# Kernel tuning notes

Measured on AMD Instinct MI355X. Metric: run time of the kernel, lower is better.

Reference implementation:

```python
import jax, jax.numpy as jnp
import numpy as np

N_NODES = 100000
N_EDGES = 1600000
IN_CH = 256
OUT_CH = 128


def setup_inputs() -> dict:
    key = jax.random.key(0)
    k1, k2, k3, k4, k5, k6 = jax.random.split(key, 6)
    x = jax.random.normal(k1, (N_NODES, IN_CH), dtype=jnp.float32)
    edge_src = jax.random.randint(k2, (N_EDGES,), 0, N_NODES, dtype=jnp.int32)
    edge_dst = jax.random.randint(k3, (N_EDGES,), 0, N_NODES, dtype=jnp.int32)
    edge_weight = jax.random.uniform(k4, (N_EDGES,), dtype=jnp.float32)
    # Linear params (torch nn.Linear: y = x @ W.T + b)
    W = jax.random.normal(k5, (OUT_CH, IN_CH), dtype=jnp.float32) * (1.0 / np.sqrt(IN_CH))
    b = jax.random.normal(k6, (OUT_CH,), dtype=jnp.float32) * 0.01
    return {"x": x, "edge_src": edge_src, "edge_dst": edge_dst,
            "edge_weight": edge_weight, "W": W, "b": b}


def reference(x, edge_src, edge_dst, edge_weight, W, b):
    # Linear projection: [N, in] -> [N, out]
    h = x @ W.T + b
    # spmm sum aggregation: out[d] = sum_{e: dst(e)=d} w_e * h[src(e)]
    msgs = h[edge_src] * edge_weight[:, None]  # [E, out]
    out = jax.ops.segment_sum(msgs, edge_dst, num_segments=N_NODES)
    return out
```

## Files before the change

### kernel.cpp

```cpp
#include <hip/hip_runtime.h>
#include <hip/hip_bf16.h>

#define IN_CH 256
#define OUT_CH 128
#define BIN_SHIFT 6
#define BIN_SIZE 64
#define MAXNB2 2048
#define CHUNK3 4096
#define NBLK_MAX 512
#define K4BATCH 1536
#define K4CAP 2048

using bf16x8 = __attribute__((ext_vector_type(8))) __bf16;
using f32x16 = __attribute__((ext_vector_type(16))) float;
using f32x4  = __attribute__((ext_vector_type(4))) float;
using f32x2  = __attribute__((ext_vector_type(2))) float;

__device__ __forceinline__ unsigned int f2bf(float f) {
    union { float f; unsigned u; } v; v.f = f;
    unsigned r = v.u + 0x7fffu + ((v.u >> 16) & 1u);
    return r >> 16;
}

__global__ void __launch_bounds__(512) k1_hist(
    const float* __restrict__ W, unsigned short* __restrict__ Wfrag,
    const int* __restrict__ edge_dst, unsigned short* __restrict__ bh,
    int n_edges, int nb2) {
    const int t = threadIdx.x;
    if (blockIdx.x < 8) {
        const int flat = blockIdx.x * 512 + t;
        const int l = flat & 63;
        const int ks = (flat >> 6) & 15;
        const int c = flat >> 10;
        const int row = c * 32 + (l & 31);
        const int col0 = ks * 16 + 8 * (l >> 5);
        const float* src = W + (size_t)row * IN_CH + col0;
        uint4 o;
        o.x = f2bf(src[0]) | (f2bf(src[1]) << 16);
        o.y = f2bf(src[2]) | (f2bf(src[3]) << 16);
        o.z = f2bf(src[4]) | (f2bf(src[5]) << 16);
        o.w = f2bf(src[6]) | (f2bf(src[7]) << 16);
        *reinterpret_cast<uint4*>(Wfrag + (size_t)flat * 8) = o;
        return;
    }
    __shared__ int hist[MAXNB2];
    const int blk = blockIdx.x - 8;
    for (int i = t; i < MAXNB2; i += 512) hist[i] = 0;
    __syncthreads();
    const int base = blk * CHUNK3;
#pragma unroll
    for (int j = 0; j < CHUNK3 / 512; ++j) {
        int e = base + j * 512 + t;
        if (e < n_edges) atomicAdd(&hist[edge_dst[e] >> BIN_SHIFT], 1);
    }
    __syncthreads();
    for (int i = t; i < nb2; i += 512) bh[(size_t)i * NBLK_MAX + blk] = (unsigned short)hist[i];
}

__global__ void __launch_bounds__(512) k2a_scan_cols(
    const unsigned short* __restrict__ bh, unsigned short* __restrict__ offs,
    int* __restrict__ total, int nblk) {
    __shared__ int sd[512];
    const int t = threadIdx.x;
    const int bin = blockIdx.x;
    int val = (t < nblk) ? (int)bh[(size_t)bin * NBLK_MAX + t] : 0;
    sd[t] = val;
    __syncthreads();
    for (int s = 1; s < 512; s <<= 1) {
        int y = (t >= s) ? sd[t - s] : 0;
        __syncthreads();
        sd[t] += y;
        __syncthreads();
    }
    offs[(size_t)bin * NBLK_MAX + t] = (unsigned short)(sd[t] - val);
    if (t == 511) total[bin] = sd[511];
}

__global__ void __launch_bounds__(512) k2b_scan_base(
    const int* __restrict__ total, int* __restrict__ base, int nb2) {
    __shared__ int sd[512];
    const int t = threadIdx.x;
    int v[4];
    int loc = 0;
#pragma unroll
    for (int k = 0; k < 4; ++k) {
        int idx = t * 4 + k;
        v[k] = (idx < nb2) ? total[idx] : 0;
        loc += v[k];
    }
    sd[t] = loc;
    __syncthreads();
    for (int s = 1; s < 512; s <<= 1) {
        int y = (t >= s) ? sd[t - s] : 0;
        __syncthreads();
        sd[t] += y;
        __syncthreads();
    }
    int run = sd[t] - loc;
#pragma unroll
    for (int k = 0; k < 4; ++k) {
        int idx = t * 4 + k;
        if (idx < nb2) base[idx] = run;
        run += v[k];
    }
    if (t == 511) base[nb2] = sd[511];
}

__global__ void __launch_bounds__(512) linear_mfma(
    const float* __restrict__ x, const unsigned short* __restrict__ Wfrag,
    const float* __restrict__ b, unsigned short* __restrict__ h, int n_nodes) {
    __shared__ uint4 wlds[4096];
    const int tid = threadIdx.x;
    const int w = tid >> 6, l = tid & 63;
    const int l31 = l & 31, lh = l >> 5;
    const int node0 = blockIdx.x * 256 + w * 32;

    {
        const uint4* wfg = reinterpret_cast<const uint4*>(Wfrag);
#pragma unroll
        for (int j = 0; j < 8; ++j) wlds[j * 512 + tid] = wfg[j * 512 + tid];
    }
    __syncthreads();

    int arow = node0 + l31;
    if (arow > n_nodes - 1) arow = n_nodes - 1;
    const float* xrow = x + (size_t)arow * IN_CH + 8 * lh;

    f32x16 acc0 = {}, acc1 = {}, acc2 = {}, acc3 = {};

#pragma unroll 4
    for (int ks = 0; ks < 16; ++ks) {
        float4 a0 = *reinterpret_cast<const float4*>(xrow + ks * 16);
        float4 a1 = *reinterpret_cast<const float4*>(xrow + ks * 16 + 4);
        bf16x8 af;
        af[0] = (__bf16)a0.x; af[1] = (__bf16)a0.y;
        af[2] = (__bf16)a0.z; af[3] = (__bf16)a0.w;
        af[4] = (__bf16)a1.x; af[5] = (__bf16)a1.y;
        af[6] = (__bf16)a1.z; af[7] = (__bf16)a1.w;

        uint4 bw0 = wlds[(0 * 16 + ks) * 64 + l];
        uint4 bw1 = wlds[(1 * 16 + ks) * 64 + l];
        uint4 bw2 = wlds[(2 * 16 + ks) * 64 + l];
        uint4 bw3 = wlds[(3 * 16 + ks) * 64 + l];

        acc0 = __builtin_amdgcn_mfma_f32_32x32x16_bf16(af, __builtin_bit_cast(bf16x8, bw0), acc0, 0, 0, 0);
        acc1 = __builtin_amdgcn_mfma_f32_32x32x16_bf16(af, __builtin_bit_cast(bf16x8, bw1), acc1, 0, 0, 0);
        acc2 = __builtin_amdgcn_mfma_f32_32x32x16_bf16(af, __builtin_bit_cast(bf16x8, bw2), acc2, 0, 0, 0);
        acc3 = __builtin_amdgcn_mfma_f32_32x32x16_bf16(af, __builtin_bit_cast(bf16x8, bw3), acc3, 0, 0, 0);
    }

    const float bias0 = b[0 + l31], bias1 = b[32 + l31], bias2 = b[64 + l31], bias3 = b[96 + l31];
#pragma unroll
    for (int reg = 0; reg < 16; ++reg) {
        const int r = (reg & 3) + 8 * (reg >> 2) + 4 * lh;
        const int node = node0 + r;
        if (node < n_nodes) {
            unsigned short* hp = h + (size_t)node * OUT_CH;
            __bf16 t0 = (__bf16)(acc0[reg] + bias0);
            __bf16 t1 = (__bf16)(acc1[reg] + bias1);
            __bf16 t2 = (__bf16)(acc2[reg] + bias2);
            __bf16 t3 = (__bf16)(acc3[reg] + bias3);
            hp[0 + l31]  = __builtin_bit_cast(unsigned short, t0);
            hp[32 + l31] = __builtin_bit_cast(unsigned short, t1);
            hp[64 + l31] = __builtin_bit_cast(unsigned short, t2);
            hp[96 + l31] = __builtin_bit_cast(unsigned short, t3);
        }
    }
}

__global__ void __launch_bounds__(512) k3_bin(
    const int* __restrict__ edge_src, const int* __restrict__ edge_dst,
    const float* __restrict__ edge_weight,
    const unsigned short* __restrict__ offs, const int* __restrict__ base,
    unsigned long long* __restrict__ records, int n_edges, int nb2) {
    __shared__ unsigned long long staged[CHUNK3];
    __shared__ int hist[MAXNB2];
    __shared__ int cur[MAXNB2];
    __shared__ int gbase[MAXNB2];
    __shared__ int sd[512];

    const int t = threadIdx.x;
    const int blk = blockIdx.x;
    const int ebase = blk * CHUNK3;
    const int count = min(CHUNK3, n_edges - ebase);

    for (int i = t; i < MAXNB2; i += 512) hist[i] = 0;
    __syncthreads();
#pragma unroll
    for (int j = 0; j < CHUNK3 / 512; ++j) {
        int e = ebase + j * 512 + t;
        if (e < n_edges) atomicAdd(&hist[edge_dst[e] >> BIN_SHIFT], 1);
    }
    __syncthreads();
    int h0 = hist[4 * t], h1 = hist[4 * t + 1], h2 = hist[4 * t + 2], h3 = hist[4 * t + 3];
    int loc = h0 + h1 + h2 + h3;
    sd[t] = loc;
    __syncthreads();
    for (int s = 1; s < 512; s <<= 1) {
        int y = (t >= s) ? sd[t - s] : 0;
        __syncthreads();
        sd[t] += y;
        __syncthreads();
    }
    int excl = sd[t] - loc;
    {
        int run = excl;
        cur[4 * t] = run; run += h0;
        cur[4 * t + 1] = run; run += h1;
        cur[4 * t + 2] = run; run += h2;
        cur[4 * t + 3] = run;
    }
    {
        int run = excl;
#pragma unroll
        for (int k = 0; k < 4; ++k) {
            int bin = 4 * t + k;
            if (bin < nb2)
                gbase[bin] = base[bin] + (int)offs[(size_t)bin * NBLK_MAX + blk] - run;
            run += (k == 0 ? h0 : k == 1 ? h1 : k == 2 ? h2 : h3);
        }
    }
    __syncthreads();
#pragma unroll
    for (int j = 0; j < CHUNK3 / 512; ++j) {
        int e = ebase + j * 512 + t;
        if (e < n_edges) {
            int d = edge_dst[e];
            int bin = d >> BIN_SHIFT;
            unsigned int wbits = f2bf(edge_weight[e]);
            unsigned long long rec = ((unsigned long long)wbits << 48) |
                                     ((unsigned long long)bin << 24) |
                                     ((unsigned long long)(d & (BIN_SIZE - 1)) << 17) |
                                     (unsigned int)edge_src[e];
            int pos = atomicAdd(&cur[bin], 1);
            staged[pos] = rec;
        }
    }
    __syncthreads();
    for (int i = t; i < count; i += 512) {
        unsigned long long r = staged[i];
        int bin = (int)((r >> 24) & 4095u);
        records[gbase[bin] + i] = r;
    }
}

__global__ void __launch_bounds__(256) k4_agg(
    const unsigned short* __restrict__ h, const unsigned long long* __restrict__ records,
    const int* __restrict__ base, float* __restrict__ out, int n_nodes) {
    __shared__ unsigned long long sorted[K4CAP];
    __shared__ int hist[BIN_SIZE];
    __shared__ int cur[BIN_SIZE];
    __shared__ int pstart[BIN_SIZE];
    __shared__ int sd[BIN_SIZE];
    __shared__ int ptot;

    const int t = threadIdx.x;
    const int bin = blockIdx.x;
    const int w = t >> 6, lane = t & 63;
    const int rbeg = base[bin], rend = base[bin + 1];

    float acc[16][2];
#pragma unroll
    for (int d = 0; d < 16; ++d) { acc[d][0] = 0.f; acc[d][1] = 0.f; }

    for (int b0 = rbeg; b0 < rend; b0 += K4BATCH) {
        const int cnt = min(K4BATCH, rend - b0);
        __syncthreads();
        if (t < BIN_SIZE) hist[t] = 0;
        __syncthreads();
        for (int i = t; i < cnt; i += 256)
            atomicAdd(&hist[(unsigned)(records[b0 + i] >> 17) & 63u], 1);
        __syncthreads();
        if (t < BIN_SIZE) sd[t] = (hist[t] + 7) & ~7;
        __syncthreads();
        for (int s = 1; s < BIN_SIZE; s <<= 1) {
            int y = 0;
            if (t < BIN_SIZE && t >= s) y = sd[t - s];
            __syncthreads();
            if (t < BIN_SIZE) sd[t] += y;
            __syncthreads();
        }
        if (t < BIN_SIZE) {
            const int e = sd[t] - ((hist[t] + 7) & ~7);
            pstart[t] = e;
            cur[t] = e;
        }
        if (t == BIN_SIZE - 1) ptot = sd[BIN_SIZE - 1];
        __syncthreads();
        const int pt = ptot;
        for (int i = t; i < pt; i += 256) sorted[i] = 0ull;
        __syncthreads();
        for (int i = t; i < cnt; i += 256) {
            const unsigned long long r = records[b0 + i];
            const int dl = (int)((unsigned)(r >> 17) & 63u);
            const int pos = atomicAdd(&cur[dl], 1);
            sorted[pos] = r;
        }
        __syncthreads();
#pragma unroll
        for (int d = 0; d < 16; ++d) {
            const int dl = w * 16 + d;
            const int s0 = pstart[dl];
            const int s1 = s0 + hist[dl];
            float a0 = 0.f, a1 = 0.f;
            for (int i = s0; i < s1; i += 8) {
                unsigned int hv[8];
                float wt[8];
#pragma unroll
                for (int j = 0; j < 8; ++j) {
                    const unsigned long long rr = sorted[i + j];
                    const unsigned lo = __builtin_amdgcn_readfirstlane((unsigned)rr);
                    const unsigned hi = __builtin_amdgcn_readfirstlane((unsigned)(rr >> 32));
                    wt[j] = __builtin_bit_cast(float, hi & 0xFFFF0000u);
                    const unsigned* hp = reinterpret_cast<const unsigned*>(
                        h + (size_t)(lo & 0x1FFFFu) * OUT_CH);
                    hv[j] = hp[lane];
                }
#pragma unroll
                for (int j = 0; j < 8; ++j) {
                    a0 += wt[j] * __builtin_bit_cast(float, hv[j] << 16);
                    a1 += wt[j] * __builtin_bit_cast(float, hv[j] & 0xFFFF0000u);
                }
            }
            acc[d][0] += a0;
            acc[d][1] += a1;
        }
    }

#pragma unroll
    for (int d = 0; d < 16; ++d) {
        const int node = bin * BIN_SIZE + w * 16 + d;
        if (node < n_nodes) {
            f32x2 v = {acc[d][0], acc[d][1]};
            __builtin_nontemporal_store(
                v, reinterpret_cast<f32x2*>(out + (size_t)node * OUT_CH + 2 * lane));
        }
    }
}

extern "C" void kernel_launch(void* const* d_in, const int* in_sizes, int n_in,
                              void* d_out, int out_size, void* d_ws, size_t ws_size,
                              hipStream_t stream) {
    const float* x           = (const float*)d_in[0];
    const int*   edge_src    = (const int*)d_in[1];
    const int*   edge_dst    = (const int*)d_in[2];
    const float* edge_weight = (const float*)d_in[3];
    const float* W           = (const float*)d_in[4];
    const float* b           = (const float*)d_in[5];
    float* out = (float*)d_out;

    const int n_nodes = in_sizes[0] / IN_CH;
    const int n_edges = in_sizes[1];
    const int nb2 = (n_nodes + BIN_SIZE - 1) / BIN_SIZE;
    const int nblk = (n_edges + CHUNK3 - 1) / CHUNK3;

    unsigned long long* records = (unsigned long long*)d_ws;
    unsigned short* h     = (unsigned short*)(records + n_edges);
    unsigned short* bh    = (unsigned short*)(h + (size_t)n_nodes * OUT_CH);
    unsigned short* offs  = bh + (size_t)MAXNB2 * NBLK_MAX;
    int* total = (int*)(offs + (size_t)MAXNB2 * NBLK_MAX);
    int* base  = total + MAXNB2;
    unsigned short* Wfrag = (unsigned short*)(base + MAXNB2 + 2);

    k1_hist<<<8 + nblk, 512, 0, stream>>>(W, Wfrag, edge_dst, bh, n_edges, nb2);
    k2a_scan_cols<<<nb2, 512, 0, stream>>>(bh, offs, total, nblk);
    k2b_scan_base<<<1, 512, 0, stream>>>(total, base, nb2);
    linear_mfma<<<(n_nodes + 255) / 256, 512, 0, stream>>>(x, Wfrag, b, h, n_nodes);
    k3_bin<<<nblk, 512, 0, stream>>>(edge_src, edge_dst, edge_weight,
                                     offs, base, records, n_edges, nb2);
    k4_agg<<<nb2, 256, 0, stream>>>(h, records, base, out, n_nodes);
}
```

Before: 135.6 us.

## Merge edge binning and linear projection into one heterogeneous launch; stage records in LDS

The edge-binning kernel and the MFMA linear projection become one launch, with the block index choosing which role a block plays. Both roles share a 64KB LDS buffer. The aim is to remove a launch boundary and let the memory-bound scatter overlap with the GEMM. Separately, the aggregation kernel now copies each record batch into LDS once instead of reading it from global memory twice. The trade-off is higher LDS use per block, which could lower occupancy.

```diff
diff --git a/kernel.cpp b/kernel.cpp
--- a/kernel.cpp
+++ b/kernel.cpp
@@ -106,19 +106,97 @@
     if (t == 511) base[nb2] = sd[511];
 }
 
-__global__ void __launch_bounds__(512) linear_mfma(
+__global__ void __launch_bounds__(512) k3_linear(
+    const int* __restrict__ edge_src, const int* __restrict__ edge_dst,
+    const float* __restrict__ edge_weight,
+    const unsigned short* __restrict__ offs, const int* __restrict__ base,
+    unsigned long long* __restrict__ records, int n_edges, int nb2, int nblk,
     const float* __restrict__ x, const unsigned short* __restrict__ Wfrag,
     const float* __restrict__ b, unsigned short* __restrict__ h, int n_nodes) {
-    __shared__ uint4 wlds[4096];
-    const int tid = threadIdx.x;
-    const int w = tid >> 6, l = tid & 63;
+    __shared__ __align__(16) char smem[65536];
+    const int t = threadIdx.x;
+
+    if ((int)blockIdx.x < nblk) {
+        unsigned long long* staged = (unsigned long long*)smem;
+        int* hist  = (int*)(smem + 32768);
+        int* cur   = (int*)(smem + 40960);
+        int* gbase = (int*)(smem + 49152);
+        int* sd    = (int*)(smem + 57344);
+
+        const int blk = blockIdx.x;
+        const int ebase = blk * CHUNK3;
+        const int count = min(CHUNK3, n_edges - ebase);
+
+        for (int i = t; i < MAXNB2; i += 512) hist[i] = 0;
+        __syncthreads();
+#pragma unroll
+        for (int j = 0; j < CHUNK3 / 512; ++j) {
+            int e = ebase + j * 512 + t;
+            if (e < n_edges) atomicAdd(&hist[edge_dst[e] >> BIN_SHIFT], 1);
+        }
+        __syncthreads();
+        int h0 = hist[4 * t], h1 = hist[4 * t + 1], h2 = hist[4 * t + 2], h3 = hist[4 * t + 3];
+        int loc = h0 + h1 + h2 + h3;
+        sd[t] = loc;
+        __syncthreads();
+        for (int s = 1; s < 512; s <<= 1) {
+            int y = (t >= s) ? sd[t - s] : 0;
+            __syncthreads();
+            sd[t] += y;
+            __syncthreads();
+        }
+        int excl = sd[t] - loc;
+        {
+            int run = excl;
+            cur[4 * t] = run; run += h0;
+            cur[4 * t + 1] = run; run += h1;
+            cur[4 * t + 2] = run; run += h2;
+            cur[4 * t + 3] = run;
+        }
+        {
+            int run = excl;
+#pragma unroll
+            for (int k = 0; k < 4; ++k) {
+                int bin = 4 * t + k;
+                if (bin < nb2)
+                    gbase[bin] = base[bin] + (int)offs[(size_t)bin * NBLK_MAX + blk] - run;
+                run += (k == 0 ? h0 : k == 1 ? h1 : k == 2 ? h2 : h3);
+            }
+        }
+        __syncthreads();
+#pragma unroll
+        for (int j = 0; j < CHUNK3 / 512; ++j) {
+            int e = ebase + j * 512 + t;
+            if (e < n_edges) {
+                int d = edge_dst[e];
+                int bin = d >> BIN_SHIFT;
+                unsigned int wbits = f2bf(edge_weight[e]);
+                unsigned long long rec = ((unsigned long long)wbits << 48) |
+                                         ((unsigned long long)bin << 24) |
+                                         ((unsigned long long)(d & (BIN_SIZE - 1)) << 17) |
+                                         (unsigned int)edge_src[e];
+                int pos = atomicAdd(&cur[bin], 1);
+                staged[pos] = rec;
+            }
+        }
+        __syncthreads();
+        for (int i = t; i < count; i += 512) {
+            unsigned long long r = staged[i];
+            int bin = (int)((r >> 24) & 4095u);
+            records[gbase[bin] + i] = r;
+        }
+        return;
+    }
+
+    uint4* wlds = (uint4*)smem;
+    const int w = t >> 6, l = t & 63;
     const int l31 = l & 31, lh = l >> 5;
-    const int node0 = blockIdx.x * 256 + w * 32;
+    const int node0 = (blockIdx.x - nblk) * 256 + w * 32;
 
     {
         const uint4* wfg = reinterpret_cast<const uint4*>(Wfrag);
 #pragma unroll
-        for (int j = 0; j < 8; ++j) wlds[j * 512 + tid] = wfg[j * 512 + tid];
+        for (int j = 0; j < 8; ++j) wlds[j * 512 + t] = wfg[j * 512 + t];
     }
     __syncthreads();
 
@@ -168,86 +246,11 @@
     }
 }
 
-__global__ void __launch_bounds__(512) k3_bin(
-    const int* __restrict__ edge_src, const int* __restrict__ edge_dst,
-    const float* __restrict__ edge_weight,
-    const unsigned short* __restrict__ offs, const int* __restrict__ base,
-    unsigned long long* __restrict__ records, int n_edges, int nb2) {
-    __shared__ unsigned long long staged[CHUNK3];
-    __shared__ int hist[MAXNB2];
-    __shared__ int cur[MAXNB2];
-    __shared__ int gbase[MAXNB2];
-    __shared__ int sd[512];
-
-    const int t = threadIdx.x;
-    const int blk = blockIdx.x;
-    const int ebase = blk * CHUNK3;
-    const int count = min(CHUNK3, n_edges - ebase);
-
-    for (int i = t; i < MAXNB2; i += 512) hist[i] = 0;
-    __syncthreads();
-#pragma unroll
-    for (int j = 0; j < CHUNK3 / 512; ++j) {
-        int e = ebase + j * 512 + t;
-        if (e < n_edges) atomicAdd(&hist[edge_dst[e] >> BIN_SHIFT], 1);
-    }
-    __syncthreads();
-    int h0 = hist[4 * t], h1 = hist[4 * t + 1], h2 = hist[4 * t + 2], h3 = hist[4 * t + 3];
-    int loc = h0 + h1 + h2 + h3;
-    sd[t] = loc;
-    __syncthreads();
-    for (int s = 1; s < 512; s <<= 1) {
-        int y = (t >= s) ? sd[t - s] : 0;
-        __syncthreads();
-        sd[t] += y;
-        __syncthreads();
-    }
-    int excl = sd[t] - loc;
-    {
-        int run = excl;
-        cur[4 * t] = run; run += h0;
-        cur[4 * t + 1] = run; run += h1;
-        cur[4 * t + 2] = run; run += h2;
-        cur[4 * t + 3] = run;
-    }
-    {
-        int run = excl;
-#pragma unroll
-        for (int k = 0; k < 4; ++k) {
-            int bin = 4 * t + k;
-            if (bin < nb2)
-                gbase[bin] = base[bin] + (int)offs[(size_t)bin * NBLK_MAX + blk] - run;
-            run += (k == 0 ? h0 : k == 1 ? h1 : k == 2 ? h2 : h3);
-        }
-    }
-    __syncthreads();
-#pragma unroll
-    for (int j = 0; j < CHUNK3 / 512; ++j) {
-        int e = ebase + j * 512 + t;
-        if (e < n_edges) {
-            int d = edge_dst[e];
-            int bin = d >> BIN_SHIFT;
-            unsigned int wbits = f2bf(edge_weight[e]);
-            unsigned long long rec = ((unsigned long long)wbits << 48) |
-                                     ((unsigned long long)bin << 24) |
-                                     ((unsigned long long)(d & (BIN_SIZE - 1)) << 17) |
-                                     (unsigned int)edge_src[e];
-            int pos = atomicAdd(&cur[bin], 1);
-            staged[pos] = rec;
-        }
-    }
-    __syncthreads();
-    for (int i = t; i < count; i += 512) {
-        unsigned long long r = staged[i];
-        int bin = (int)((r >> 24) & 4095u);
-        records[gbase[bin] + i] = r;
-    }
-}
-
 __global__ void __launch_bounds__(256) k4_agg(
     const unsigned short* __restrict__ h, const unsigned long long* __restrict__ records,
     const int* __restrict__ base, float* __restrict__ out, int n_nodes) {
     __shared__ unsigned long long sorted[K4CAP];
+    __shared__ unsigned long long staged[K4BATCH];
     __shared__ int hist[BIN_SIZE];
     __shared__ int cur[BIN_SIZE];
     __shared__ int pstart[BIN_SIZE];
@@ -266,10 +269,11 @@
     for (int b0 = rbeg; b0 < rend; b0 += K4BATCH) {
         const int cnt = min(K4BATCH, rend - b0);
         __syncthreads();
+        for (int i = t; i < cnt; i += 256) staged[i] = records[b0 + i];
         if (t < BIN_SIZE) hist[t] = 0;
         __syncthreads();
         for (int i = t; i < cnt; i += 256)
-            atomicAdd(&hist[(unsigned)(records[b0 + i] >> 17) & 63u], 1);
+            atomicAdd(&hist[(unsigned)(staged[i] >> 17) & 63u], 1);
         __syncthreads();
         if (t < BIN_SIZE) sd[t] = (hist[t] + 7) & ~7;
         __syncthreads();
@@ -291,7 +295,7 @@
         for (int i = t; i < pt; i += 256) sorted[i] = 0ull;
         __syncthreads();
         for (int i = t; i < cnt; i += 256) {
-            const unsigned long long r = records[b0 + i];
+            const unsigned long long r = staged[i];
             const int dl = (int)((unsigned)(r >> 17) & 63u);
             const int pos = atomicAdd(&cur[dl], 1);
             sorted[pos] = r;
@@ -353,6 +357,7 @@
     const int n_edges = in_sizes[1];
     const int nb2 = (n_nodes + BIN_SIZE - 1) / BIN_SIZE;
     const int nblk = (n_edges + CHUNK3 - 1) / CHUNK3;
+    const int lblocks = (n_nodes + 255) / 256;
 
     unsigned long long* records = (unsigned long long*)d_ws;
     unsigned short* h     = (unsigned short*)(records + n_edges);
@@ -365,8 +370,8 @@
     k1_hist<<<8 + nblk, 512, 0, stream>>>(W, Wfrag, edge_dst, bh, n_edges, nb2);
     k2a_scan_cols<<<nb2, 512, 0, stream>>>(bh, offs, total, nblk);
     k2b_scan_base<<<1, 512, 0, stream>>>(total, base, nb2);
-    linear_mfma<<<(n_nodes + 255) / 256, 512, 0, stream>>>(x, Wfrag, b, h, n_nodes);
-    k3_bin<<<nblk, 512, 0, stream>>>(edge_src, edge_dst, edge_weight,
-                                     offs, base, records, n_edges, nb2);
+    k3_linear<<<nblk + lblocks, 512, 0, stream>>>(
+        edge_src, edge_dst, edge_weight, offs, base, records, n_edges, nb2, nblk,
+        x, Wfrag, b, h, n_nodes);
     k4_agg<<<nb2, 256, 0, stream>>>(h, records, base, out, n_nodes);
 }
```

Result: faster. 131.3 us (-3.2%).

## Fuse linear projection into histogram kernel and stage k4 records in LDS

Applied to the files above, without the earlier changes.

Merges the MFMA linear projection into the edge-histogram kernel. Each linear block converts W to bf16 fragments itself, which removes the separate Wfrag pass and one kernel launch, and lets the GEMM overlap with histogram blocks. In k4_agg, each batch of records is loaded once into shared memory instead of being read twice from global memory, and the 64-entry scan uses wavefront shuffles instead of a barrier-heavy LDS scan. In exchange, every linear block redundantly converts W, and the fused kernel reserves 64KB of LDS for all blocks, which may reduce histogram-block occupancy.

```diff
diff --git a/kernel.cpp b/kernel.cpp
--- a/kernel.cpp
+++ b/kernel.cpp
@@ -22,29 +22,89 @@
     return r >> 16;
 }
 
-__global__ void __launch_bounds__(512) k1_hist(
-    const float* __restrict__ W, unsigned short* __restrict__ Wfrag,
-    const int* __restrict__ edge_dst, unsigned short* __restrict__ bh,
-    int n_edges, int nb2) {
-    const int t = threadIdx.x;
-    if (blockIdx.x < 8) {
-        const int flat = blockIdx.x * 512 + t;
-        const int l = flat & 63;
-        const int ks = (flat >> 6) & 15;
-        const int c = flat >> 10;
-        const int row = c * 32 + (l & 31);
-        const int col0 = ks * 16 + 8 * (l >> 5);
-        const float* src = W + (size_t)row * IN_CH + col0;
-        uint4 o;
-        o.x = f2bf(src[0]) | (f2bf(src[1]) << 16);
-        o.y = f2bf(src[2]) | (f2bf(src[3]) << 16);
-        o.z = f2bf(src[4]) | (f2bf(src[5]) << 16);
-        o.w = f2bf(src[6]) | (f2bf(src[7]) << 16);
-        *reinterpret_cast<uint4*>(Wfrag + (size_t)flat * 8) = o;
+__global__ void __launch_bounds__(512) k1_linear(
+    const float* __restrict__ W, const int* __restrict__ edge_dst,
+    unsigned short* __restrict__ bh, int n_edges, int nb2,
+    const float* __restrict__ x, const float* __restrict__ b,
+    unsigned short* __restrict__ h, int n_nodes, int lblocks) {
+    __shared__ __align__(16) char smem[65536];
+    const int t = threadIdx.x;
+
+    if ((int)blockIdx.x < lblocks) {
+        uint4* wlds = (uint4*)smem;
+        const int w = t >> 6, l = t & 63;
+        const int l31 = l & 31, lh = l >> 5;
+        const int node0 = blockIdx.x * 256 + w * 32;
+
+#pragma unroll
+        for (int j = 0; j < 8; ++j) {
+            const int flat = j * 512 + t;
+            const int fl = flat & 63;
+            const int ks = (flat >> 6) & 15;
+            const int c = flat >> 10;
+            const int row = c * 32 + (fl & 31);
+            const int col0 = ks * 16 + 8 * (fl >> 5);
+            const float* src = W + (size_t)row * IN_CH + col0;
+            float4 s0 = *reinterpret_cast<const float4*>(src);
+            float4 s1 = *reinterpret_cast<const float4*>(src + 4);
+            uint4 o;
+            o.x = f2bf(s0.x) | (f2bf(s0.y) << 16);
+            o.y = f2bf(s0.z) | (f2bf(s0.w) << 16);
+            o.z = f2bf(s1.x) | (f2bf(s1.y) << 16);
+            o.w = f2bf(s1.z) | (f2bf(s1.w) << 16);
+            wlds[flat] = o;
+        }
+        __syncthreads();
+
+        int arow = node0 + l31;
+        if (arow > n_nodes - 1) arow = n_nodes - 1;
+        const float* xrow = x + (size_t)arow * IN_CH + 8 * lh;
+
+        f32x16 acc0 = {}, acc1 = {}, acc2 = {}, acc3 = {};
+
+#pragma unroll 4
+        for (int ks = 0; ks < 16; ++ks) {
+            float4 a0 = *reinterpret_cast<const float4*>(xrow + ks * 16);
+            float4 a1 = *reinterpret_cast<const float4*>(xrow + ks * 16 + 4);
+            bf16x8 af;
+            af[0] = (__bf16)a0.x; af[1] = (__bf16)a0.y;
+            af[2] = (__bf16)a0.z; af[3] = (__bf16)a0.w;
+            af[4] = (__bf16)a1.x; af[5] = (__bf16)a1.y;
+            af[6] = (__bf16)a1.z; af[7] = (__bf16)a1.w;
+
+            uint4 bw0 = wlds[(0 * 16 + ks) * 64 + l];
+            uint4 bw1 = wlds[(1 * 16 + ks) * 64 + l];
+            uint4 bw2 = wlds[(2 * 16 + ks) * 64 + l];
+            uint4 bw3 = wlds[(3 * 16 + ks) * 64 + l];
+
+            acc0 = __builtin_amdgcn_mfma_f32_32x32x16_bf16(af, __builtin_bit_cast(bf16x8, bw0), acc0, 0, 0, 0);
+            acc1 = __builtin_amdgcn_mfma_f32_32x32x16_bf16(af, __builtin_bit_cast(bf16x8, bw1), acc1, 0, 0, 0);
+            acc2 = __builtin_amdgcn_mfma_f32_32x32x16_bf16(af, __builtin_bit_cast(bf16x8, bw2), acc2, 0, 0, 0);
+            acc3 = __builtin_amdgcn_mfma_f32_32x32x16_bf16(af, __builtin_bit_cast(bf16x8, bw3), acc3, 0, 0, 0);
+        }
+
+        const float bias0 = b[0 + l31], bias1 = b[32 + l31], bias2 = b[64 + l31], bias3 = b[96 + l31];
+#pragma unroll
+        for (int reg = 0; reg < 16; ++reg) {
+            const int r = (reg & 3) + 8 * (reg >> 2) + 4 * lh;
+            const int node = node0 + r;
+            if (node < n_nodes) {
+                unsigned short* hp = h + (size_t)node * OUT_CH;
+                __bf16 t0 = (__bf16)(acc0[reg] + bias0);
+                __bf16 t1 = (__bf16)(acc1[reg] + bias1);
+                __bf16 t2 = (__bf16)(acc2[reg] + bias2);
+                __bf16 t3 = (__bf16)(acc3[reg] + bias3);
+                hp[0 + l31]  = __builtin_bit_cast(unsigned short, t0);
+                hp[32 + l31] = __builtin_bit_cast(unsigned short, t1);
+                hp[64 + l31] = __builtin_bit_cast(unsigned short, t2);
+                hp[96 + l31] = __builtin_bit_cast(unsigned short, t3);
+            }
+        }
         return;
     }
-    __shared__ int hist[MAXNB2];
-    const int blk = blockIdx.x - 8;
+
+    int* hist = (int*)smem;
+    const int blk = blockIdx.x - lblocks;
     for (int i = t; i < MAXNB2; i += 512) hist[i] = 0;
     __syncthreads();
     const int base = blk * CHUNK3;
@@ -104,68 +164,6 @@
         run += v[k];
     }
     if (t == 511) base[nb2] = sd[511];
-}
-
-__global__ void __launch_bounds__(512) linear_mfma(
-    const float* __restrict__ x, const unsigned short* __restrict__ Wfrag,
-    const float* __restrict__ b, unsigned short* __restrict__ h, int n_nodes) {
-    __shared__ uint4 wlds[4096];
-    const int tid = threadIdx.x;
-    const int w = tid >> 6, l = tid & 63;
-    const int l31 = l & 31, lh = l >> 5;
-    const int node0 = blockIdx.x * 256 + w * 32;
-
-    {
-        const uint4* wfg = reinterpret_cast<const uint4*>(Wfrag);
-#pragma unroll
-        for (int j = 0; j < 8; ++j) wlds[j * 512 + tid] = wfg[j * 512 + tid];
-    }
-    __syncthreads();
-
-    int arow = node0 + l31;
-    if (arow > n_nodes - 1) arow = n_nodes - 1;
-    const float* xrow = x + (size_t)arow * IN_CH + 8 * lh;
-
-    f32x16 acc0 = {}, acc1 = {}, acc2 = {}, acc3 = {};
-
-#pragma unroll 4
-    for (int ks = 0; ks < 16; ++ks) {
-        float4 a0 = *reinterpret_cast<const float4*>(xrow + ks * 16);
-        float4 a1 = *reinterpret_cast<const float4*>(xrow + ks * 16 + 4);
-        bf16x8 af;
-        af[0] = (__bf16)a0.x; af[1] = (__bf16)a0.y;
-        af[2] = (__bf16)a0.z; af[3] = (__bf16)a0.w;
-        af[4] = (__bf16)a1.x; af[5] = (__bf16)a1.y;
-        af[6] = (__bf16)a1.z; af[7] = (__bf16)a1.w;
-
-        uint4 bw0 = wlds[(0 * 16 + ks) * 64 + l];
-        uint4 bw1 = wlds[(1 * 16 + ks) * 64 + l];
-        uint4 bw2 = wlds[(2 * 16 + ks) * 64 + l];
-        uint4 bw3 = wlds[(3 * 16 + ks) * 64 + l];
-
-        acc0 = __builtin_amdgcn_mfma_f32_32x32x16_bf16(af, __builtin_bit_cast(bf16x8, bw0), acc0, 0, 0, 0);
-        acc1 = __builtin_amdgcn_mfma_f32_32x32x16_bf16(af, __builtin_bit_cast(bf16x8, bw1), acc1, 0, 0, 0);
-        acc2 = __builtin_amdgcn_mfma_f32_32x32x16_bf16(af, __builtin_bit_cast(bf16x8, bw2), acc2, 0, 0, 0);
-        acc3 = __builtin_amdgcn_mfma_f32_32x32x16_bf16(af, __builtin_bit_cast(bf16x8, bw3), acc3, 0, 0, 0);
-    }
-
-    const float bias0 = b[0 + l31], bias1 = b[32 + l31], bias2 = b[64 + l31], bias3 = b[96 + l31];
-#pragma unroll
-    for (int reg = 0; reg < 16; ++reg) {
-        const int r = (reg & 3) + 8 * (reg >> 2) + 4 * lh;
-        const int node = node0 + r;
-        if (node < n_nodes) {
-            unsigned short* hp = h + (size_t)node * OUT_CH;
-            __bf16 t0 = (__bf16)(acc0[reg] + bias0);
-            __bf16 t1 = (__bf16)(acc1[reg] + bias1);
-            __bf16 t2 = (__bf16)(acc2[reg] + bias2);
-            __bf16 t3 = (__bf16)(acc3[reg] + bias3);
-            hp[0 + l31]  = __builtin_bit_cast(unsigned short, t0);
-            hp[32 + l31] = __builtin_bit_cast(unsigned short, t1);
-            hp[64 + l31] = __builtin_bit_cast(unsigned short, t2);
-            hp[96 + l31] = __builtin_bit_cast(unsigned short, t3);
-        }
-    }
 }
 
 __global__ void __launch_bounds__(512) k3_bin(
@@ -248,10 +246,10 @@
     const unsigned short* __restrict__ h, const unsigned long long* __restrict__ records,
     const int* __restrict__ base, float* __restrict__ out, int n_nodes) {
     __shared__ unsigned long long sorted[K4CAP];
+    __shared__ unsigned long long staged[K4BATCH];
     __shared__ int hist[BIN_SIZE];
     __shared__ int cur[BIN_SIZE];
     __shared__ int pstart[BIN_SIZE];
-    __shared__ int sd[BIN_SIZE];
     __shared__ int ptot;
 
     const int t = threadIdx.x;
@@ -266,32 +264,30 @@
     for (int b0 = rbeg; b0 < rend; b0 += K4BATCH) {
         const int cnt = min(K4BATCH, rend - b0);
         __syncthreads();
+        for (int i = t; i < cnt; i += 256) staged[i] = records[b0 + i];
         if (t < BIN_SIZE) hist[t] = 0;
         __syncthreads();
         for (int i = t; i < cnt; i += 256)
-            atomicAdd(&hist[(unsigned)(records[b0 + i] >> 17) & 63u], 1);
-        __syncthreads();
-        if (t < BIN_SIZE) sd[t] = (hist[t] + 7) & ~7;
-        __syncthreads();
-        for (int s = 1; s < BIN_SIZE; s <<= 1) {
-            int y = 0;
-            if (t < BIN_SIZE && t >= s) y = sd[t - s];
-            __syncthreads();
-            if (t < BIN_SIZE) sd[t] += y;
-            __syncthreads();
-        }
+            atomicAdd(&hist[(unsigned)(staged[i] >> 17) & 63u], 1);
+        __syncthreads();
         if (t < BIN_SIZE) {
-            const int e = sd[t] - ((hist[t] + 7) & ~7);
-            pstart[t] = e;
-            cur[t] = e;
-        }
-        if (t == BIN_SIZE - 1) ptot = sd[BIN_SIZE - 1];
+            const int v = (hist[t] + 7) & ~7;
+            int s = v;
+#pragma unroll
+            for (int st = 1; st < 64; st <<= 1) {
+                int y = __shfl_up(s, st);
+                if (t >= st) s += y;
+            }
+            pstart[t] = s - v;
+            cur[t] = s - v;
+            if (t == 63) ptot = s;
+        }
         __syncthreads();
         const int pt = ptot;
         for (int i = t; i < pt; i += 256) sorted[i] = 0ull;
         __syncthreads();
         for (int i = t; i < cnt; i += 256) {
-            const unsigned long long r = records[b0 + i];
+            const unsigned long long r = staged[i];
             const int dl = (int)((unsigned)(r >> 17) & 63u);
             const int pos = atomicAdd(&cur[dl], 1);
             sorted[pos] = r;
@@ -353,6 +349,7 @@
     const int n_edges = in_sizes[1];
     const int nb2 = (n_nodes + BIN_SIZE - 1) / BIN_SIZE;
     const int nblk = (n_edges + CHUNK3 - 1) / CHUNK3;
+    const int lblocks = (n_nodes + 255) / 256;
 
     unsigned long long* records = (unsigned long long*)d_ws;
     unsigned short* h     = (unsigned short*)(records + n_edges);
@@ -360,12 +357,11 @@
     unsigned short* offs  = bh + (size_t)MAXNB2 * NBLK_MAX;
     int* total = (int*)(offs + (size_t)MAXNB2 * NBLK_MAX);
     int* base  = total + MAXNB2;
-    unsigned short* Wfrag = (unsigned short*)(base + MAXNB2 + 2);
-
-    k1_hist<<<8 + nblk, 512, 0, stream>>>(W, Wfrag, edge_dst, bh, n_edges, nb2);
+
+    k1_linear<<<lblocks + nblk, 512, 0, stream>>>(
+        W, edge_dst, bh, n_edges, nb2, x, b, h, n_nodes, lblocks);
     k2a_scan_cols<<<nb2, 512, 0, stream>>>(bh, offs, total, nblk);
     k2b_scan_base<<<1, 512, 0, stream>>>(total, base, nb2);
-    linear_mfma<<<(n_nodes + 255) / 256, 512, 0, stream>>>(x, Wfrag, b, h, n_nodes);
     k3_bin<<<nblk, 512, 0, stream>>>(edge_src, edge_dst, edge_weight,
                                      offs, base, records, n_edges, nb2);
     k4_agg<<<nb2, 256, 0, stream>>>(h, records, base, out, n_nodes);
```

Result: faster. 131.2 us (median of 2 runs) (-3.2%).
